# Kernel optimization log

Hardware: AMD Instinct MI355X
Metric: run time of the kernel (lower is better)

## Reference

```python
import jax, jax.numpy as jnp
import numpy as np

B, H, N, D = 4, 16, 2048, 64

def setup_inputs() -> dict:
    key = jax.random.key(0)
    kq, kk, kv = jax.random.split(key, 3)
    q = jax.random.normal(kq, (B, H, N, D), dtype=jnp.float32)
    k = jax.random.normal(kk, (B, H, N, D), dtype=jnp.float32)
    v = jax.random.normal(kv, (B, H, N, D), dtype=jnp.float32)
    return {"q": q, "k": k, "v": v}

def reference(q, k, v):
    scale = q.shape[-1] ** -0.5
    # sim: [b, h, i, j]
    sim = jnp.einsum('bhid,bhjd->bhij', q, k) * scale
    attn = jax.nn.softmax(sim, axis=-1)  # dropout p=0.0 -> identity
    out = jnp.einsum('bhij,bhjd->bhid', attn, v)
    return out
```

## Files before the change

### kernel.cpp

```cpp
#include <hip/hip_runtime.h>
#include <stdint.h>


#define NSEQ 2048
#define DH   64
#define BHN  64
#define BM   128
#define BN   64
#define NIT  (NSEQ / BN)

typedef short bf16x8 __attribute__((ext_vector_type(8)));
typedef float f32x4  __attribute__((ext_vector_type(4)));
typedef float f32x16 __attribute__((ext_vector_type(16)));

__device__ __forceinline__ uint16_t f2bf(float x) {
    uint32_t u = __builtin_bit_cast(uint32_t, x);
    return (uint16_t)((u + 0x7fffu + ((u >> 16) & 1u)) >> 16);
}
__device__ __forceinline__ uint32_t pk2(float a, float b) {
    return (uint32_t)f2bf(a) | ((uint32_t)f2bf(b) << 16);
}
__device__ __forceinline__ void gload_lds16(const uint16_t* g, uint16_t* l) {
    __builtin_amdgcn_global_load_lds(
        (const __attribute__((address_space(1))) uint32_t*)g,
        (__attribute__((address_space(3))) uint32_t*)l, 16, 0, 0);
}

__global__ __launch_bounds__(256) void prepass(const float* __restrict__ K,
                                               const float* __restrict__ V,
                                               uint16_t* __restrict__ Kb,
                                               uint16_t* __restrict__ Vt) {
    __shared__ float T[64 * 68];
    int b = blockIdx.x;
    if (b < 4096) {
        size_t i = ((size_t)b * 256 + threadIdx.x) * 8;
        float4 a = *(const float4*)(K + i);
        float4 c = *(const float4*)(K + i + 4);
        *(uint4*)(Kb + i) = make_uint4(pk2(a.x, a.y), pk2(a.z, a.w),
                                       pk2(c.x, c.y), pk2(c.z, c.w));
        return;
    }
    b -= 4096;
    const int t  = threadIdx.x;
    const int bh = b >> 5;
    const int n0 = (b & 31) * 64;
    const float* vb = V + (size_t)bh * NSEQ * DH + (size_t)n0 * DH;
    {
        const int n = t >> 4, d0 = (t & 15) * 4;
        #pragma unroll
        for (int p = 0; p < 4; ++p)
            *(float4*)&T[(n + 16 * p) * 68 + d0] =
                *(const float4*)(vb + (size_t)(n + 16 * p) * DH + d0);
    }
    __syncthreads();
    const int d = t >> 2;
    #pragma unroll
    for (int q = 0; q < 2; ++q) {
        const int oct = (t & 3) + 4 * q;
        const int g = oct >> 1, ib = (oct & 1) * 8;
        float f[8];
        #pragma unroll
        for (int j = 0; j < 8; ++j) {
            int i = ib + j;
            int s = (i & 3) + 8 * ((i >> 2) & 1) + 4 * ((i >> 3) & 1);
            f[j] = T[(g * 16 + s) * 68 + d];
        }
        uint4 o = make_uint4(pk2(f[0], f[1]), pk2(f[2], f[3]),
                             pk2(f[4], f[5]), pk2(f[6], f[7]));
        *(uint4*)(Vt + ((size_t)bh * DH + d) * NSEQ + n0 + oct * 8) = o;
    }
}

__global__ __launch_bounds__(128) void attn_main(const float* __restrict__ Qg,
                                                 const uint16_t* __restrict__ Kb,
                                                 const uint16_t* __restrict__ Vt,
                                                 float* __restrict__ Og) {
    __shared__ __align__(16) uint16_t Ks[BN * DH];
    __shared__ __align__(16) uint16_t Vs[DH * BN];
    __shared__ float Lb[BM];

    const int tid = threadIdx.x;
    const int w = tid >> 6, lane = tid & 63, l31 = lane & 31, h = lane >> 5;
    const int bh = blockIdx.x >> 4;
    const int qt = blockIdx.x & 15;

    const float qscale = 0.125f * 1.44269504f;
    bf16x8 qf[2][4];
    #pragma unroll
    for (int nt = 0; nt < 2; ++nt) {
        const float* qp = Qg + ((size_t)bh * NSEQ +
                                (size_t)(qt * BM + w * 64 + nt * 32 + l31)) * DH + h * 8;
        #pragma unroll
        for (int k2 = 0; k2 < 4; ++k2) {
            float4 a = *(const float4*)(qp + k2 * 16);
            float4 c = *(const float4*)(qp + k2 * 16 + 4);
            union { uint32_t u[4]; bf16x8 v; } pk;
            pk.u[0] = pk2(a.x * qscale, a.y * qscale);
            pk.u[1] = pk2(a.z * qscale, a.w * qscale);
            pk.u[2] = pk2(c.x * qscale, c.y * qscale);
            pk.u[3] = pk2(c.z * qscale, c.w * qscale);
            qf[nt][k2] = pk.v;
        }
    }

    f32x16 oacc[2][2] = {};
    float lsum[2] = {0.0f, 0.0f};

    const int rr = w * 32 + (lane >> 3);
    const int cc = (lane & 7) ^ (lane >> 3);
    const uint16_t* gK = Kb + (size_t)bh * NSEQ * DH + (size_t)rr * DH + cc * 8;
    const uint16_t* gV = Vt + (size_t)bh * DH * NSEQ + (size_t)rr * NSEQ + cc * 8;
    uint16_t* lK = &Ks[w * 2048];
    uint16_t* lV = &Vs[w * 2048];

    #pragma unroll 1
    for (int kt = 0; kt < NIT; ++kt) {
        __syncthreads();
        #pragma unroll
        for (int i = 0; i < 4; ++i) {
            gload_lds16(gK + (size_t)i * 8 * DH,   lK + i * 512);
            gload_lds16(gV + (size_t)i * 8 * NSEQ, lV + i * 512);
        }
        gK += BN * DH;
        gV += BN;
        __syncthreads();

        #pragma unroll
        for (int mtj = 0; mtj < 2; ++mtj) {
            bf16x8 kf[4];
            #pragma unroll
            for (int k2 = 0; k2 < 4; ++k2) {
                int row = mtj * 32 + l31, c = k2 * 2 + h;
                kf[k2] = *(const bf16x8*)&Ks[row * 64 + (c ^ (row & 7)) * 8];
            }
            bf16x8 vfl[2][2];
            #pragma unroll
            for (int ktl = 0; ktl < 2; ++ktl)
                #pragma unroll
                for (int nd = 0; nd < 2; ++nd) {
                    int row = nd * 32 + l31, c = (2 * mtj + ktl) * 2 + h;
                    vfl[ktl][nd] = *(const bf16x8*)&Vs[row * 64 + (c ^ (row & 7)) * 8];
                }
            #pragma unroll
            for (int nt = 0; nt < 2; ++nt) {
                f32x16 s = {};
                #pragma unroll
                for (int k2 = 0; k2 < 4; ++k2)
                    s = __builtin_amdgcn_mfma_f32_32x32x16_bf16(kf[k2], qf[nt][k2], s, 0, 0, 0);
                bf16x8 pf[2];
                float ls = 0.0f;
                #pragma unroll
                for (int ktl = 0; ktl < 2; ++ktl) {
                    union { uint32_t u[4]; bf16x8 v; } pp;
                    #pragma unroll
                    for (int t2 = 0; t2 < 4; ++t2) {
                        float e0 = __builtin_amdgcn_exp2f(s[ktl * 8 + 2 * t2]);
                        float e1 = __builtin_amdgcn_exp2f(s[ktl * 8 + 2 * t2 + 1]);
                        ls += e0 + e1;
                        pp.u[t2] = __builtin_amdgcn_perm(
                            __builtin_bit_cast(uint32_t, e1),
                            __builtin_bit_cast(uint32_t, e0), 0x07060302u);
                    }
                    pf[ktl] = pp.v;
                }
                lsum[nt] += ls;
                #pragma unroll
                for (int nd = 0; nd < 2; ++nd) {
                    oacc[nt][nd] = __builtin_amdgcn_mfma_f32_32x32x16_bf16(pf[0], vfl[0][nd], oacc[nt][nd], 0, 0, 0);
                    oacc[nt][nd] = __builtin_amdgcn_mfma_f32_32x32x16_bf16(pf[1], vfl[1][nd], oacc[nt][nd], 0, 0, 0);
                }
            }
        }
    }

    lsum[0] += __shfl_xor(lsum[0], 32);
    lsum[1] += __shfl_xor(lsum[1], 32);
    if (h == 0) {
        Lb[w * 64 + l31]      = lsum[0];
        Lb[w * 64 + 32 + l31] = lsum[1];
    }
    float* Ob = Og + (size_t)bh * NSEQ * DH;
    #pragma unroll
    for (int nt = 0; nt < 2; ++nt) {
        float inv[16];
        #pragma unroll
        for (int rg = 0; rg < 16; ++rg) {
            int il = (rg & 3) + 8 * (rg >> 2) + 4 * h;
            inv[rg] = 1.0f / Lb[w * 64 + nt * 32 + il];
        }
        #pragma unroll
        for (int nd = 0; nd < 2; ++nd)
            #pragma unroll
            for (int rg = 0; rg < 16; ++rg) {
                int il  = (rg & 3) + 8 * (rg >> 2) + 4 * h;
                int row = qt * BM + w * 64 + nt * 32 + il;
                Ob[(size_t)row * DH + nd * 32 + l31] = oacc[nt][nd][rg] * inv[rg];
            }
    }
}

#define LDS_S 72
#define NWAVE 4
__global__ __launch_bounds__(256) void attn_fwd_fb(const float* __restrict__ Qg,
                                                   const float* __restrict__ Kg,
                                                   const float* __restrict__ Vg,
                                                   float* __restrict__ Og) {
    __shared__ short KsF[BN * LDS_S];
    __shared__ short VtsF[DH * LDS_S];
    __shared__ short PsF[NWAVE * 16 * LDS_S];
    const int tid = threadIdx.x;
    const int wave = tid >> 6, lane = tid & 63, quad = lane >> 4, l16 = lane & 15;
    const int bh = blockIdx.x >> 5, qtf = blockIdx.x & 31;
    const size_t base = (size_t)bh * NSEQ * DH;
    const float* Qb = Qg + base; const float* Kbf = Kg + base;
    const float* Vb = Vg + base; float* Ob = Og + base;
    const float qscale = 0.125f * 1.44269504f;
    bf16x8 qfrag[2];
    {
        const int qrow = qtf * 64 + wave * 16 + l16;
        const float* qp = Qb + (size_t)qrow * DH + quad * 8;
        #pragma unroll
        for (int c = 0; c < 2; ++c) {
            float4 x = *(const float4*)(qp + 32 * c);
            float4 y = *(const float4*)(qp + 32 * c + 4);
            union { uint16_t u[8]; bf16x8 v; } pk;
            pk.u[0]=f2bf(x.x*qscale); pk.u[1]=f2bf(x.y*qscale);
            pk.u[2]=f2bf(x.z*qscale); pk.u[3]=f2bf(x.w*qscale);
            pk.u[4]=f2bf(y.x*qscale); pk.u[5]=f2bf(y.y*qscale);
            pk.u[6]=f2bf(y.z*qscale); pk.u[7]=f2bf(y.w*qscale);
            qfrag[c] = pk.v;
        }
    }
    f32x4 o[4] = {};
    float m_i[4], l_i[4];
    #pragma unroll
    for (int r = 0; r < 4; ++r) { m_i[r] = -1e30f; l_i[r] = 0.0f; }
    const int kr0 = tid >> 4, kd0 = (tid & 15) * 4;
    const int vp = (tid & 31) * 2, vd0 = (tid >> 5) * 8;
    #pragma unroll 1
    for (int kt = 0; kt < NSEQ / BN; ++kt) {
        __syncthreads();
        {
            const float* kbase = Kbf + (size_t)kt * BN * DH;
            #pragma unroll
            for (int jj = 0; jj < 4; ++jj) {
                const int row = kr0 + jj * 16;
                float4 x = *(const float4*)(kbase + (size_t)row * DH + kd0);
                union { uint16_t u[4]; uint64_t ll; } pk;
                pk.u[0]=f2bf(x.x); pk.u[1]=f2bf(x.y); pk.u[2]=f2bf(x.z); pk.u[3]=f2bf(x.w);
                *(uint64_t*)&KsF[row * LDS_S + kd0] = pk.ll;
            }
        }
        {
            const float* v0 = Vb + (size_t)(kt * BN + vp) * DH + vd0;
            const float* v1 = v0 + DH;
            float4 a0 = *(const float4*)(v0); float4 a1 = *(const float4*)(v0 + 4);
            float4 b0 = *(const float4*)(v1); float4 b1 = *(const float4*)(v1 + 4);
            float av[8] = {a0.x,a0.y,a0.z,a0.w,a1.x,a1.y,a1.z,a1.w};
            float bv[8] = {b0.x,b0.y,b0.z,b0.w,b1.x,b1.y,b1.z,b1.w};
            #pragma unroll
            for (int i = 0; i < 8; ++i)
                *(uint32_t*)&VtsF[(vd0 + i) * LDS_S + vp] = pk2(av[i], bv[i]);
        }
        __syncthreads();
        f32x4 s[4] = {};
        #pragma unroll
        for (int c = 0; c < 2; ++c)
            #pragma unroll
            for (int n = 0; n < 4; ++n) {
                bf16x8 kfr = *(const bf16x8*)&KsF[(n * 16 + l16) * LDS_S + quad * 8 + 32 * c];
                s[n] = __builtin_amdgcn_mfma_f32_16x16x32_bf16(qfrag[c], kfr, s[n], 0, 0, 0);
            }
        float rmax[4];
        #pragma unroll
        for (int r = 0; r < 4; ++r)
            rmax[r] = fmaxf(fmaxf(s[0][r], s[1][r]), fmaxf(s[2][r], s[3][r]));
        #pragma unroll
        for (int off = 1; off < 16; off <<= 1)
            #pragma unroll
            for (int r = 0; r < 4; ++r)
                rmax[r] = fmaxf(rmax[r], __shfl_xor(rmax[r], off, 64));
        float alpha[4], rsum[4];
        #pragma unroll
        for (int r = 0; r < 4; ++r) {
            float mn = fmaxf(m_i[r], rmax[r]);
            alpha[r] = __builtin_amdgcn_exp2f(m_i[r] - mn);
            m_i[r] = mn; rsum[r] = 0.0f;
        }
        #pragma unroll
        for (int n = 0; n < 4; ++n)
            #pragma unroll
            for (int r = 0; r < 4; ++r) {
                float p = __builtin_amdgcn_exp2f(s[n][r] - m_i[r]);
                rsum[r] += p;
                PsF[(wave * 16 + quad * 4 + r) * LDS_S + n * 16 + l16] = (short)f2bf(p);
            }
        #pragma unroll
        for (int off = 1; off < 16; off <<= 1)
            #pragma unroll
            for (int r = 0; r < 4; ++r)
                rsum[r] += __shfl_xor(rsum[r], off, 64);
        #pragma unroll
        for (int r = 0; r < 4; ++r) l_i[r] = l_i[r] * alpha[r] + rsum[r];
        #pragma unroll
        for (int n = 0; n < 4; ++n)
            #pragma unroll
            for (int r = 0; r < 4; ++r) o[n][r] *= alpha[r];
        #pragma unroll
        for (int c = 0; c < 2; ++c) {
            bf16x8 pfr = *(const bf16x8*)&PsF[(wave * 16 + l16) * LDS_S + quad * 8 + 32 * c];
            #pragma unroll
            for (int n = 0; n < 4; ++n) {
                bf16x8 vfr = *(const bf16x8*)&VtsF[(n * 16 + l16) * LDS_S + quad * 8 + 32 * c];
                o[n] = __builtin_amdgcn_mfma_f32_16x16x32_bf16(pfr, vfr, o[n], 0, 0, 0);
            }
        }
    }
    float inv[4];
    #pragma unroll
    for (int r = 0; r < 4; ++r) inv[r] = 1.0f / l_i[r];
    const int orow0 = qtf * 64 + wave * 16 + quad * 4;
    #pragma unroll
    for (int n = 0; n < 4; ++n)
        #pragma unroll
        for (int r = 0; r < 4; ++r)
            Ob[(size_t)(orow0 + r) * DH + n * 16 + l16] = o[n][r] * inv[r];
}

extern "C" void kernel_launch(void* const* d_in, const int* in_sizes, int n_in,
                              void* d_out, int out_size, void* d_ws, size_t ws_size,
                              hipStream_t stream) {
    (void)in_sizes; (void)n_in; (void)out_size;
    const float* q = (const float*)d_in[0];
    const float* k = (const float*)d_in[1];
    const float* v = (const float*)d_in[2];
    float* out = (float*)d_out;
    const size_t elems = (size_t)BHN * NSEQ * DH;
    const size_t need  = 2 * elems * sizeof(uint16_t);
    if (ws_size >= need) {
        uint16_t* kb = (uint16_t*)d_ws;
        uint16_t* vt = kb + elems;
        prepass<<<dim3(4096 + BHN * (NSEQ / 64)), dim3(256), 0, stream>>>(k, v, kb, vt);
        attn_main<<<dim3(BHN * (NSEQ / BM)), dim3(128), 0, stream>>>(q, kb, vt, out);
    } else {
        attn_fwd_fb<<<dim3(BHN * (NSEQ / 64)), dim3(256), 0, stream>>>(q, k, v, out);
    }
}
```

Baseline: 225.2 us.

## Prepack K/V into MFMA fragment layout and load fragments directly from global

The prepass now writes K and V as bf16 in the exact per-lane MFMA operand order, one 16 KB block per 64-key tile. The main kernel becomes a single-wave block with no LDS and no barriers, and loads its fragments straight into registers with coalesced 16-byte loads. Block indices are remapped so that consecutive blocks cover different heads, and row sums are broadcast with ds_bpermute instead of going through LDS. In exchange each wave rereads K/V from L2/global per query tile with no sharing inside a block, and register pressure rises from holding 16 uint4 fragments per iteration.

```diff
diff --git a/kernel.cpp b/kernel.cpp
--- a/kernel.cpp
+++ b/kernel.cpp
@@ -5,9 +5,7 @@
 #define NSEQ 2048
 #define DH   64
 #define BHN  64
-#define BM   128
-#define BN   64
-#define NIT  (NSEQ / BN)
+#define NIT  32
 
 typedef short bf16x8 __attribute__((ext_vector_type(8)));
 typedef float f32x4  __attribute__((ext_vector_type(4)));
@@ -20,76 +18,63 @@
 __device__ __forceinline__ uint32_t pk2(float a, float b) {
     return (uint32_t)f2bf(a) | ((uint32_t)f2bf(b) << 16);
 }
-__device__ __forceinline__ void gload_lds16(const uint16_t* g, uint16_t* l) {
-    __builtin_amdgcn_global_load_lds(
-        (const __attribute__((address_space(1))) uint32_t*)g,
-        (__attribute__((address_space(3))) uint32_t*)l, 16, 0, 0);
-}
 
 __global__ __launch_bounds__(256) void prepass(const float* __restrict__ K,
                                                const float* __restrict__ V,
-                                               uint16_t* __restrict__ Kb,
-                                               uint16_t* __restrict__ Vt) {
-    __shared__ float T[64 * 68];
-    int b = blockIdx.x;
-    if (b < 4096) {
-        size_t i = ((size_t)b * 256 + threadIdx.x) * 8;
-        float4 a = *(const float4*)(K + i);
-        float4 c = *(const float4*)(K + i + 4);
-        *(uint4*)(Kb + i) = make_uint4(pk2(a.x, a.y), pk2(a.z, a.w),
-                                       pk2(c.x, c.y), pk2(c.z, c.w));
-        return;
-    }
-    b -= 4096;
-    const int t  = threadIdx.x;
-    const int bh = b >> 5;
-    const int n0 = (b & 31) * 64;
-    const float* vb = V + (size_t)bh * NSEQ * DH + (size_t)n0 * DH;
-    {
-        const int n = t >> 4, d0 = (t & 15) * 4;
-        #pragma unroll
-        for (int p = 0; p < 4; ++p)
-            *(float4*)&T[(n + 16 * p) * 68 + d0] =
-                *(const float4*)(vb + (size_t)(n + 16 * p) * DH + d0);
+                                               uint16_t* __restrict__ F) {
+    __shared__ float T0[64 * 68];
+    __shared__ float T1[64 * 68];
+    const int b = blockIdx.x, bh = b >> 5, kt = b & 31, t = threadIdx.x;
+    const size_t gbase = ((size_t)bh * NSEQ + (size_t)kt * 64) * DH;
+    const int n = t >> 2, d0 = (t & 3) * 16;
+    #pragma unroll
+    for (int i = 0; i < 4; ++i) {
+        *(float4*)&T0[n * 68 + d0 + i * 4] = *(const float4*)(K + gbase + n * 64 + d0 + i * 4);
+        *(float4*)&T1[n * 68 + d0 + i * 4] = *(const float4*)(V + gbase + n * 64 + d0 + i * 4);
     }
     __syncthreads();
-    const int d = t >> 2;
-    #pragma unroll
-    for (int q = 0; q < 2; ++q) {
-        const int oct = (t & 3) + 4 * q;
-        const int g = oct >> 1, ib = (oct & 1) * 8;
+    uint16_t* out = F + (size_t)(bh * 32 + kt) * 8192;
+    #pragma unroll
+    for (int p = 0; p < 4; ++p) {
+        const int e = p * 256 + t, c = e >> 6, l = e & 63;
+        const int ll = l & 31, hh = l >> 5;
         float f[8];
-        #pragma unroll
-        for (int j = 0; j < 8; ++j) {
-            int i = ib + j;
-            int s = (i & 3) + 8 * ((i >> 2) & 1) + 4 * ((i >> 3) & 1);
-            f[j] = T[(g * 16 + s) * 68 + d];
+        if (c < 8) {
+            const int row = (c >> 2) * 32 + ll;
+            const int col = hh * 8 + (c & 3) * 16;
+            #pragma unroll
+            for (int j = 0; j < 8; ++j) f[j] = T0[row * 68 + col + j];
+        } else {
+            const int cc = c - 8, ktg = cc >> 1;
+            const int d = (cc & 1) * 32 + ll;
+            #pragma unroll
+            for (int j = 0; j < 8; ++j) {
+                const int i = hh * 8 + j;
+                const int s = (i & 3) + 8 * ((i >> 2) & 1) + 4 * ((i >> 3) & 1);
+                f[j] = T1[(ktg * 16 + s) * 68 + d];
+            }
         }
         uint4 o = make_uint4(pk2(f[0], f[1]), pk2(f[2], f[3]),
                              pk2(f[4], f[5]), pk2(f[6], f[7]));
-        *(uint4*)(Vt + ((size_t)bh * DH + d) * NSEQ + n0 + oct * 8) = o;
-    }
-}
-
-__global__ __launch_bounds__(128) void attn_main(const float* __restrict__ Qg,
-                                                 const uint16_t* __restrict__ Kb,
-                                                 const uint16_t* __restrict__ Vt,
-                                                 float* __restrict__ Og) {
-    __shared__ __align__(16) uint16_t Ks[BN * DH];
-    __shared__ __align__(16) uint16_t Vs[DH * BN];
-    __shared__ float Lb[BM];
-
-    const int tid = threadIdx.x;
-    const int w = tid >> 6, lane = tid & 63, l31 = lane & 31, h = lane >> 5;
-    const int bh = blockIdx.x >> 4;
-    const int qt = blockIdx.x & 15;
+        *(uint4*)(out + (size_t)c * 512 + l * 8) = o;
+    }
+}
+
+__global__ __launch_bounds__(64, 2) void attn_main(const float* __restrict__ Qg,
+                                                   const uint16_t* __restrict__ F,
+                                                   float* __restrict__ Og) {
+    const int lane = threadIdx.x;
+    const int l31 = lane & 31, h = lane >> 5;
+    const int idx = blockIdx.x;
+    const int bh = (idx & 7) * 8 + ((idx >> 3) & 7);
+    const int qt = idx >> 6;
 
     const float qscale = 0.125f * 1.44269504f;
     bf16x8 qf[2][4];
     #pragma unroll
     for (int nt = 0; nt < 2; ++nt) {
         const float* qp = Qg + ((size_t)bh * NSEQ +
-                                (size_t)(qt * BM + w * 64 + nt * 32 + l31)) * DH + h * 8;
+                                (size_t)(qt * 64 + nt * 32 + l31)) * DH + h * 8;
         #pragma unroll
         for (int k2 = 0; k2 < 4; ++k2) {
             float4 a = *(const float4*)(qp + k2 * 16);
@@ -106,47 +91,26 @@
     f32x16 oacc[2][2] = {};
     float lsum[2] = {0.0f, 0.0f};
 
-    const int rr = w * 32 + (lane >> 3);
-    const int cc = (lane & 7) ^ (lane >> 3);
-    const uint16_t* gK = Kb + (size_t)bh * NSEQ * DH + (size_t)rr * DH + cc * 8;
-    const uint16_t* gV = Vt + (size_t)bh * DH * NSEQ + (size_t)rr * NSEQ + cc * 8;
-    uint16_t* lK = &Ks[w * 2048];
-    uint16_t* lV = &Vs[w * 2048];
+    const uint16_t* fb = F + (size_t)bh * 32 * 8192 + (size_t)lane * 8;
 
     #pragma unroll 1
     for (int kt = 0; kt < NIT; ++kt) {
-        __syncthreads();
-        #pragma unroll
-        for (int i = 0; i < 4; ++i) {
-            gload_lds16(gK + (size_t)i * 8 * DH,   lK + i * 512);
-            gload_lds16(gV + (size_t)i * 8 * NSEQ, lV + i * 512);
-        }
-        gK += BN * DH;
-        gV += BN;
-        __syncthreads();
+        uint4 kc[8], vc[8];
+        #pragma unroll
+        for (int c = 0; c < 8; ++c) kc[c] = *(const uint4*)(fb + (size_t)c * 512);
+        #pragma unroll
+        for (int c = 0; c < 8; ++c) vc[c] = *(const uint4*)(fb + (size_t)(8 + c) * 512);
+        fb += 8192;
 
         #pragma unroll
         for (int mtj = 0; mtj < 2; ++mtj) {
-            bf16x8 kf[4];
-            #pragma unroll
-            for (int k2 = 0; k2 < 4; ++k2) {
-                int row = mtj * 32 + l31, c = k2 * 2 + h;
-                kf[k2] = *(const bf16x8*)&Ks[row * 64 + (c ^ (row & 7)) * 8];
-            }
-            bf16x8 vfl[2][2];
-            #pragma unroll
-            for (int ktl = 0; ktl < 2; ++ktl)
-                #pragma unroll
-                for (int nd = 0; nd < 2; ++nd) {
-                    int row = nd * 32 + l31, c = (2 * mtj + ktl) * 2 + h;
-                    vfl[ktl][nd] = *(const bf16x8*)&Vs[row * 64 + (c ^ (row & 7)) * 8];
-                }
             #pragma unroll
             for (int nt = 0; nt < 2; ++nt) {
                 f32x16 s = {};
                 #pragma unroll
                 for (int k2 = 0; k2 < 4; ++k2)
-                    s = __builtin_amdgcn_mfma_f32_32x32x16_bf16(kf[k2], qf[nt][k2], s, 0, 0, 0);
+                    s = __builtin_amdgcn_mfma_f32_32x32x16_bf16(
+                        __builtin_bit_cast(bf16x8, kc[mtj * 4 + k2]), qf[nt][k2], s, 0, 0, 0);
                 bf16x8 pf[2];
                 float ls = 0.0f;
                 #pragma unroll
@@ -166,41 +130,39 @@
                 lsum[nt] += ls;
                 #pragma unroll
                 for (int nd = 0; nd < 2; ++nd) {
-                    oacc[nt][nd] = __builtin_amdgcn_mfma_f32_32x32x16_bf16(pf[0], vfl[0][nd], oacc[nt][nd], 0, 0, 0);
-                    oacc[nt][nd] = __builtin_amdgcn_mfma_f32_32x32x16_bf16(pf[1], vfl[1][nd], oacc[nt][nd], 0, 0, 0);
+                    oacc[nt][nd] = __builtin_amdgcn_mfma_f32_32x32x16_bf16(
+                        pf[0], __builtin_bit_cast(bf16x8, vc[(2 * mtj + 0) * 2 + nd]),
+                        oacc[nt][nd], 0, 0, 0);
+                    oacc[nt][nd] = __builtin_amdgcn_mfma_f32_32x32x16_bf16(
+                        pf[1], __builtin_bit_cast(bf16x8, vc[(2 * mtj + 1) * 2 + nd]),
+                        oacc[nt][nd], 0, 0, 0);
                 }
             }
         }
     }
 
-    lsum[0] += __shfl_xor(lsum[0], 32);
-    lsum[1] += __shfl_xor(lsum[1], 32);
-    if (h == 0) {
-        Lb[w * 64 + l31]      = lsum[0];
-        Lb[w * 64 + 32 + l31] = lsum[1];
-    }
     float* Ob = Og + (size_t)bh * NSEQ * DH;
     #pragma unroll
     for (int nt = 0; nt < 2; ++nt) {
-        float inv[16];
+        float lt = lsum[nt] + __shfl_xor(lsum[nt], 32);
+        float rinv = 1.0f / lt;
+        int rib = __builtin_bit_cast(int, rinv);
         #pragma unroll
         for (int rg = 0; rg < 16; ++rg) {
-            int il = (rg & 3) + 8 * (rg >> 2) + 4 * h;
-            inv[rg] = 1.0f / Lb[w * 64 + nt * 32 + il];
-        }
-        #pragma unroll
-        for (int nd = 0; nd < 2; ++nd)
-            #pragma unroll
-            for (int rg = 0; rg < 16; ++rg) {
-                int il  = (rg & 3) + 8 * (rg >> 2) + 4 * h;
-                int row = qt * BM + w * 64 + nt * 32 + il;
-                Ob[(size_t)row * DH + nd * 32 + l31] = oacc[nt][nd][rg] * inv[rg];
-            }
+            const int il = (rg & 3) + 8 * (rg >> 2) + 4 * h;
+            const float inv = __builtin_bit_cast(float,
+                __builtin_amdgcn_ds_bpermute(il * 4, rib));
+            const int row = qt * 64 + nt * 32 + il;
+            #pragma unroll
+            for (int nd = 0; nd < 2; ++nd)
+                Ob[(size_t)row * DH + nd * 32 + l31] = oacc[nt][nd][rg] * inv;
+        }
     }
 }
 
 #define LDS_S 72
 #define NWAVE 4
+#define BN    64
 __global__ __launch_bounds__(256) void attn_fwd_fb(const float* __restrict__ Qg,
                                                    const float* __restrict__ Kg,
                                                    const float* __restrict__ Vg,
@@ -335,14 +297,12 @@
     const float* k = (const float*)d_in[1];
     const float* v = (const float*)d_in[2];
     float* out = (float*)d_out;
-    const size_t elems = (size_t)BHN * NSEQ * DH;
-    const size_t need  = 2 * elems * sizeof(uint16_t);
+    const size_t need = (size_t)BHN * 32 * 16384;
     if (ws_size >= need) {
-        uint16_t* kb = (uint16_t*)d_ws;
-        uint16_t* vt = kb + elems;
-        prepass<<<dim3(4096 + BHN * (NSEQ / 64)), dim3(256), 0, stream>>>(k, v, kb, vt);
-        attn_main<<<dim3(BHN * (NSEQ / BM)), dim3(128), 0, stream>>>(q, kb, vt, out);
+        uint16_t* fbuf = (uint16_t*)d_ws;
+        prepass<<<dim3(BHN * 32), dim3(256), 0, stream>>>(k, v, fbuf);
+        attn_main<<<dim3(2048), dim3(64), 0, stream>>>(q, fbuf, out);
     } else {
-        attn_fwd_fb<<<dim3(BHN * (NSEQ / 64)), dim3(256), 0, stream>>>(q, k, v, out);
-    }
-}
+        attn_fwd_fb<<<dim3(BHN * 32), dim3(256), 0, stream>>>(q, k, v, out);
+    }
+}
```

Result: faster. 196.0 us (-13.0%).
